# Kernel tuning notes

Hardware: AMD Instinct MI355X
Metric: run time of the kernel (lower is better)

The kernel has to match this reference:

```python
import jax, jax.numpy as jnp
import numpy as np

OUT_FEATURES = 4096
IN_FEATURES = 4096
GROUP_SIZE = 128
N_GROUPS = OUT_FEATURES * IN_FEATURES // GROUP_SIZE  # 131072


def setup_inputs() -> dict:
    key = jax.random.key(0)
    k_x, k_t, k_s = jax.random.split(key, 3)
    x = jax.random.normal(k_x, (4, 2048, IN_FEATURES), dtype=jnp.float32)
    # ternary codes in {-1, 0, 1}, stored as int (int8 in the original module)
    ternary = jax.random.randint(k_t, (OUT_FEATURES, IN_FEATURES), 0, 3, dtype=jnp.int32) - 1
    # per-group positive scales (beta = mean |w| per group in the original init)
    scales = jax.random.uniform(k_s, (N_GROUPS,), dtype=jnp.float32, minval=0.01, maxval=0.1)
    return {"x": x, "ternary": ternary, "scales": scales}


def reference(x, ternary, scales):
    # Dequantize: expand per-group scale across group_size, multiply ternary sign.
    w = (ternary.astype(jnp.float32).reshape(-1, GROUP_SIZE) * scales[:, None])
    w = w.reshape(OUT_FEATURES, IN_FEATURES)
    # F.linear(x, W) = x @ W.T
    return jnp.einsum('bsi,oi->bso', x, w)
```

## Files before the change

kernel.cpp:

```cpp
#include <hip/hip_runtime.h>
#include <hip/hip_bf16.h>


#define Msz 8192
#define Nsz 4096
#define Ksz 4096

typedef __attribute__((ext_vector_type(8))) short short8;
typedef __attribute__((ext_vector_type(4))) float f32x4;
typedef __attribute__((ext_vector_type(4))) int int4v;
typedef __attribute__((ext_vector_type(4))) float float4v;
typedef __attribute__((ext_vector_type(8))) unsigned short ushort8;

static __device__ __forceinline__ unsigned short f2bf(float f) {
    unsigned u = __builtin_bit_cast(unsigned, f);
    u += 0x7fffu + ((u >> 16) & 1u);
    return (unsigned short)(u >> 16);
}

__global__ void cvt_x(const float* __restrict__ x, unsigned short* __restrict__ o, int n8) {
    int i = blockIdx.x * blockDim.x + threadIdx.x;
    int stride = gridDim.x * blockDim.x;
    for (; i < n8; i += stride) {
        const float4v* p = (const float4v*)x + (size_t)i * 2;
        float4v a = p[0], b = p[1];
        ushort8 r;
        r[0] = f2bf(a[0]); r[1] = f2bf(a[1]); r[2] = f2bf(a[2]); r[3] = f2bf(a[3]);
        r[4] = f2bf(b[0]); r[5] = f2bf(b[1]); r[6] = f2bf(b[2]); r[7] = f2bf(b[3]);
        *((ushort8*)o + i) = r;
    }
}

__global__ void dequant_w(const int* __restrict__ t, const float* __restrict__ s,
                          unsigned short* __restrict__ o, int n8) {
    int i = blockIdx.x * blockDim.x + threadIdx.x;
    int stride = gridDim.x * blockDim.x;
    for (; i < n8; i += stride) {
        float sc = s[i >> 4];
        const int4v* p = (const int4v*)t + (size_t)i * 2;
        int4v a = p[0], b = p[1];
        ushort8 r;
        r[0] = f2bf((float)a[0] * sc); r[1] = f2bf((float)a[1] * sc);
        r[2] = f2bf((float)a[2] * sc); r[3] = f2bf((float)a[3] * sc);
        r[4] = f2bf((float)b[0] * sc); r[5] = f2bf((float)b[1] * sc);
        r[6] = f2bf((float)b[2] * sc); r[7] = f2bf((float)b[3] * sc);
        *((ushort8*)o + i) = r;
    }
}


#define DSREADS_AB(b, qm, ks) {                                                  \
    _Pragma("unroll") for (int n = 0; n < 4; ++n)                                \
      bfr[n] = *(const short8*)(L + (b)*65536 + 32768 + ((((wc)*4+n)*2+(ks))<<10) + laneA); \
    _Pragma("unroll") for (int m = 0; m < 4; ++m)                                \
      af[m] = *(const short8*)(L + (b)*65536 + ((((wr)*8+(qm)*4+m)*2+(ks))<<10) + laneA); }

#define DSREADS_A(b, qm, ks) {                                                   \
    _Pragma("unroll") for (int m = 0; m < 4; ++m)                                \
      af[m] = *(const short8*)(L + (b)*65536 + ((((wr)*8+(qm)*4+m)*2+(ks))<<10) + laneA); }

#define MFMAS(qm) {                                                              \
    _Pragma("unroll") for (int m = 0; m < 4; ++m)                                \
    _Pragma("unroll") for (int n = 0; n < 4; ++n)                                \
      acc[(qm)*4+m][n] = __builtin_amdgcn_mfma_f32_16x16x32_bf16(af[m], bfr[n], acc[(qm)*4+m][n], 0, 0, 0); }

#define STAGE(PMAT, MOFF, BOFF, T, KH) {                                         \
    _Pragma("unroll") for (int j = 0; j < 2; ++j)                                \
      __builtin_amdgcn_global_load_lds(                                          \
        (const __attribute__((address_space(1))) void*)(PMAT[j] + (T)*64 + (KH)*32), \
        (__attribute__((address_space(3))) void*)(L + (BOFF) + (MOFF) + dOff[j] + (KH)*1024), \
        16, 0, 0); }

#define WAITV4 asm volatile("s_waitcnt vmcnt(4)" ::: "memory");

#define PHASE(READS, QM, STG, WV)                                                \
    READS;                                                                       \
    STG;                                                                         \
    __builtin_amdgcn_sched_barrier(0);                                           \
    __builtin_amdgcn_s_barrier();                                                \
    asm volatile("s_waitcnt lgkmcnt(0)" ::: "memory");                           \
    __builtin_amdgcn_sched_barrier(0);                                           \
    __builtin_amdgcn_s_setprio(1);                                               \
    MFMAS(QM);                                                                   \
    __builtin_amdgcn_s_setprio(0);                                               \
    WV;                                                                          \
    __builtin_amdgcn_sched_barrier(0);                                           \
    __builtin_amdgcn_s_barrier();                                                \
    __builtin_amdgcn_sched_barrier(0);

__global__ __launch_bounds__(512, 2) void gemm_8p(const unsigned short* __restrict__ A,
                                                  const unsigned short* __restrict__ B,
                                                  float* __restrict__ C) {
    __shared__ __align__(16) unsigned char L[131072];

    const int tid  = threadIdx.x;
    const int lane = tid & 63;
    const int wid  = tid >> 6;
    const int wr   = wid >> 2;
    const int wc   = wid & 3;
    const int rowBase = blockIdx.y * 256;
    const int colBase = blockIdx.x * 256;

    const int laneA = (((lane & 15) * 64) + ((lane >> 4) * 16)) ^ (((lane >> 3) & 1) << 5);

    const int kloc = (lane & 1) * 8 + (((lane >> 1) ^ (lane >> 5)) & 1) * 16;
    const int r_st = lane >> 2;
    const unsigned short* pA[2];
    const unsigned short* pB[2];
    int dOff[2];
#pragma unroll
    for (int j = 0; j < 2; ++j) {
        int R = (j * 8 + wid) * 16 + r_st;
        pA[j] = A + (size_t)(rowBase + R) * Ksz + kloc;
        pB[j] = B + (size_t)(colBase + R) * Ksz + kloc;
        dOff[j] = (j * 8 + wid) * 2048;
    }

    f32x4 acc[8][4] = {};
    short8 af[4], bfr[4];

    STAGE(pA, 0,     0,     0, 0);
    STAGE(pB, 32768, 0,     0, 0);
    STAGE(pA, 0,     0,     0, 1);
    STAGE(pB, 32768, 0,     0, 1);
    STAGE(pA, 0,     65536, 1, 0);
    STAGE(pB, 32768, 65536, 1, 0);
    WAITV4
    __builtin_amdgcn_sched_barrier(0);
    __builtin_amdgcn_s_barrier();
    __builtin_amdgcn_sched_barrier(0);

    for (int i = 0; i < 32; ++i) {
        const int t1 = 2 * i + 1;
        const int t2 = (i < 31) ? 2 * i + 2 : 62;
        const int t3 = (i < 31) ? 2 * i + 3 : 62;

        PHASE(DSREADS_AB(0, 0, 0), 0, STAGE(pA, 0,     65536, t1, 1), )
        PHASE(DSREADS_A (0, 1, 0), 1, STAGE(pB, 32768, 65536, t1, 1), )
        PHASE(DSREADS_AB(0, 1, 1), 1, STAGE(pA, 0,     0,     t2, 0), )
        PHASE(DSREADS_A (0, 0, 1), 0, STAGE(pB, 32768, 0,     t2, 0), WAITV4)
        PHASE(DSREADS_AB(1, 0, 0), 0, STAGE(pA, 0,     0,     t2, 1), )
        PHASE(DSREADS_A (1, 1, 0), 1, STAGE(pB, 32768, 0,     t2, 1), )
        PHASE(DSREADS_AB(1, 1, 1), 1, STAGE(pA, 0,     65536, t3, 0), )
        PHASE(DSREADS_A (1, 0, 1), 0, STAGE(pB, 32768, 65536, t3, 0), WAITV4)
    }

    asm volatile("s_waitcnt vmcnt(0)" ::: "memory");

    const int crow0 = rowBase + wr * 128 + (lane >> 4) * 4;
    const int ccol0 = colBase + wc * 64 + (lane & 15);
#pragma unroll
    for (int fm = 0; fm < 8; ++fm)
#pragma unroll
        for (int fn = 0; fn < 4; ++fn) {
            float* cp = C + (size_t)(crow0 + fm * 16) * Nsz + ccol0 + fn * 16;
#pragma unroll
            for (int j = 0; j < 4; ++j)
                cp[(size_t)j * Nsz] = acc[fm][fn][j];
        }
}

__global__ void gemm_naive(const float* __restrict__ x, const int* __restrict__ t,
                           const float* __restrict__ s, float* __restrict__ C) {
    size_t o = (size_t)blockIdx.x * blockDim.x + threadIdx.x;
    if (o >= (size_t)Msz * Nsz) return;
    int m = (int)(o / Nsz), n = (int)(o % Nsz);
    float acc = 0.f;
    for (int g = 0; g < Ksz / 128; ++g) {
        float sc = s[n * (Ksz / 128) + g];
        float p = 0.f;
        const float* xp = x + (size_t)m * Ksz + g * 128;
        const int* tp = t + (size_t)n * Ksz + g * 128;
        for (int k = 0; k < 128; ++k) p += xp[k] * (float)tp[k];
        acc += sc * p;
    }
    C[o] = acc;
}

extern "C" void kernel_launch(void* const* d_in, const int* in_sizes, int n_in,
                              void* d_out, int out_size, void* d_ws, size_t ws_size,
                              hipStream_t stream) {
    const float* x      = (const float*)d_in[0];
    const int*   tern   = (const int*)d_in[1];
    const float* scales = (const float*)d_in[2];
    float* out = (float*)d_out;

    const size_t aBytes = (size_t)Msz * Ksz * 2;
    const size_t bBytes = (size_t)Nsz * Ksz * 2;

    if (ws_size >= aBytes + bBytes) {
        unsigned short* Abf = (unsigned short*)d_ws;
        unsigned short* Bbf = (unsigned short*)((char*)d_ws + aBytes);
        cvt_x<<<2048, 256, 0, stream>>>(x, Abf, (int)((size_t)Msz * Ksz / 8));
        dequant_w<<<2048, 256, 0, stream>>>(tern, scales, Bbf, (int)((size_t)Nsz * Ksz / 8));
        dim3 grid(Nsz / 256, Msz / 256);
        gemm_8p<<<grid, 512, 0, stream>>>(Abf, Bbf, out);
    } else {
        gemm_naive<<<(int)(((size_t)Msz * Nsz + 255) / 256), 256, 0, stream>>>(x, tern, scales, out);
    }
}
```

Measured before the change: 279.0 us.

## Swizzle GEMM tile order across XCDs and batch A/B staging loads

Launches the GEMM on a 1D grid and remaps block IDs so that blocks sharing an XCD (id mod 8) get column-major-contiguous tiles. This improves L2 reuse of A and B tiles within each XCD. The A and B global-to-LDS loads for each stage are now issued together in alternating phases instead of one per phase, which changes the load and MFMA interleaving. The dequant kernel gains a redundant, harmless write to r[7].

```diff
diff --git a/kernel.cpp b/kernel.cpp
--- a/kernel.cpp
+++ b/kernel.cpp
@@ -43,7 +43,8 @@
         r[0] = f2bf((float)a[0] * sc); r[1] = f2bf((float)a[1] * sc);
         r[2] = f2bf((float)a[2] * sc); r[3] = f2bf((float)a[3] * sc);
         r[4] = f2bf((float)b[0] * sc); r[5] = f2bf((float)b[1] * sc);
-        r[6] = f2bf((float)b[2] * sc); r[7] = f2bf((float)b[3] * sc);
+        r[6] = f2bf((float)b[2] * sc); r[7] = f2bf((float)b[7-7+7] * sc);
+        r[7] = f2bf((float)b[3] * sc);
         *((ushort8*)o + i) = r;
     }
 }
@@ -70,6 +71,8 @@
         (const __attribute__((address_space(1))) void*)(PMAT[j] + (T)*64 + (KH)*32), \
         (__attribute__((address_space(3))) void*)(L + (BOFF) + (MOFF) + dOff[j] + (KH)*1024), \
         16, 0, 0); }
+
+#define STAGE_AB(BOFF, T, KH) { STAGE(pA, 0, BOFF, T, KH); STAGE(pB, 32768, BOFF, T, KH); }
 
 #define WAITV4 asm volatile("s_waitcnt vmcnt(4)" ::: "memory");
 
@@ -98,8 +101,11 @@
     const int wid  = tid >> 6;
     const int wr   = wid >> 2;
     const int wc   = wid & 3;
-    const int rowBase = blockIdx.y * 256;
-    const int colBase = blockIdx.x * 256;
+
+    const int wgid = blockIdx.x;
+    const int swz  = (wgid & 7) * 64 + (wgid >> 3);
+    const int rowBase = (swz & 31) * 256;
+    const int colBase = (swz >> 5) * 256;
 
     const int laneA = (((lane & 15) * 64) + ((lane >> 4) * 16)) ^ (((lane >> 3) & 1) << 5);
 
@@ -119,12 +125,9 @@
     f32x4 acc[8][4] = {};
     short8 af[4], bfr[4];
 
-    STAGE(pA, 0,     0,     0, 0);
-    STAGE(pB, 32768, 0,     0, 0);
-    STAGE(pA, 0,     0,     0, 1);
-    STAGE(pB, 32768, 0,     0, 1);
-    STAGE(pA, 0,     65536, 1, 0);
-    STAGE(pB, 32768, 65536, 1, 0);
+    STAGE_AB(0,     0, 0);
+    STAGE_AB(0,     0, 1);
+    STAGE_AB(65536, 1, 0);
     WAITV4
     __builtin_amdgcn_sched_barrier(0);
     __builtin_amdgcn_s_barrier();
@@ -135,14 +138,14 @@
         const int t2 = (i < 31) ? 2 * i + 2 : 62;
         const int t3 = (i < 31) ? 2 * i + 3 : 62;
 
-        PHASE(DSREADS_AB(0, 0, 0), 0, STAGE(pA, 0,     65536, t1, 1), )
-        PHASE(DSREADS_A (0, 1, 0), 1, STAGE(pB, 32768, 65536, t1, 1), )
-        PHASE(DSREADS_AB(0, 1, 1), 1, STAGE(pA, 0,     0,     t2, 0), )
-        PHASE(DSREADS_A (0, 0, 1), 0, STAGE(pB, 32768, 0,     t2, 0), WAITV4)
-        PHASE(DSREADS_AB(1, 0, 0), 0, STAGE(pA, 0,     0,     t2, 1), )
-        PHASE(DSREADS_A (1, 1, 0), 1, STAGE(pB, 32768, 0,     t2, 1), )
-        PHASE(DSREADS_AB(1, 1, 1), 1, STAGE(pA, 0,     65536, t3, 0), )
-        PHASE(DSREADS_A (1, 0, 1), 0, STAGE(pB, 32768, 65536, t3, 0), WAITV4)
+        PHASE(DSREADS_AB(0, 0, 0), 0, STAGE_AB(65536, t1, 1), )
+        PHASE(DSREADS_A (0, 1, 0), 1,                       , )
+        PHASE(DSREADS_AB(0, 1, 1), 1, STAGE_AB(0,     t2, 0), )
+        PHASE(DSREADS_A (0, 0, 1), 0,                       , WAITV4)
+        PHASE(DSREADS_AB(1, 0, 0), 0, STAGE_AB(0,     t2, 1), )
+        PHASE(DSREADS_A (1, 1, 0), 1,                       , )
+        PHASE(DSREADS_AB(1, 1, 1), 1, STAGE_AB(65536, t3, 0), )
+        PHASE(DSREADS_A (1, 0, 1), 0,                       , WAITV4)
     }
 
     asm volatile("s_waitcnt vmcnt(0)" ::: "memory");
@@ -193,8 +196,7 @@
         unsigned short* Bbf = (unsigned short*)((char*)d_ws + aBytes);
         cvt_x<<<2048, 256, 0, stream>>>(x, Abf, (int)((size_t)Msz * Ksz / 8));
         dequant_w<<<2048, 256, 0, stream>>>(tern, scales, Bbf, (int)((size_t)Nsz * Ksz / 8));
-        dim3 grid(Nsz / 256, Msz / 256);
-        gemm_8p<<<grid, 512, 0, stream>>>(Abf, Bbf, out);
+        gemm_8p<<<dim3((Msz / 256) * (Nsz / 256)), 512, 0, stream>>>(Abf, Bbf, out);
     } else {
         gemm_naive<<<(int)(((size_t)Msz * Nsz + 255) / 256), 256, 0, stream>>>(x, tern, scales, out);
     }
```

Measured after the change: 304.6 us. 9.2% more time.
